# Kernel tuning notes

Measured on AMD Instinct MI355X. Metric: run time of the kernel, lower is better.

Reference implementation:

```python
import jax, jax.numpy as jnp
import numpy as np

N_NODES = 10000
N_EDGES = 320000
D = 128      # node/edge feature dim
H = 512      # MLP hidden width


def _mlp(x, W1, b1, W2, b2):
    return jax.nn.relu(x @ W1 + b1) @ W2 + b2


def setup_inputs() -> dict:
    key = jax.random.key(0)
    ks = jax.random.split(key, 8)
    s = lambda fan_in: 1.0 / np.sqrt(fan_in)
    return {
        "x": jax.random.normal(ks[0], (N_NODES, D), jnp.float32),
        "edge_index": jax.random.randint(ks[1], (2, N_EDGES), 0, N_NODES, jnp.int64),
        "edge_attr": jax.random.normal(ks[2], (N_EDGES, D), jnp.float32),
        "We1": jax.random.normal(ks[3], (3 * D, H), jnp.float32) * s(3 * D),
        "be1": jnp.zeros((H,), jnp.float32),
        "We2": jax.random.normal(ks[4], (H, D), jnp.float32) * s(H),
        "be2": jnp.zeros((D,), jnp.float32),
        "Wn1": jax.random.normal(ks[5], (2 * D, H), jnp.float32) * s(2 * D),
        "bn1": jnp.zeros((H,), jnp.float32),
        "Wn2": jax.random.normal(ks[6], (H, D), jnp.float32) * s(H),
        "bn2": jnp.zeros((D,), jnp.float32),
    }


def reference(x, edge_index, edge_attr, We1, be1, We2, be2, Wn1, bn1, Wn2, bn2):
    senders = edge_index[0]
    receivers = edge_index[1]
    # gather -> edge MLP
    edge_inputs = jnp.concatenate([x[senders], x[receivers], edge_attr], axis=-1)  # [E, 3D]
    updated_edge_attr = _mlp(edge_inputs, We1, be1, We2, be2)                      # [E, D]
    # scatter-add into receiving nodes
    aggregated = jax.ops.segment_sum(updated_edge_attr, receivers, num_segments=x.shape[0])  # [N, D]
    # node MLP
    node_inputs = jnp.concatenate([x, aggregated], axis=-1)                        # [N, 2D]
    updated_nodes = _mlp(node_inputs, Wn1, bn1, Wn2, bn2)                          # [N, D]
    return updated_nodes, updated_edge_attr
```

## Files before the change

kernel.cpp:

```cpp
#include <hip/hip_runtime.h>
#include <hip/hip_bf16.h>

#define N_NODES 10000
#define N_EDGES 320000
#define D 128
#define H 512

typedef __bf16 bf16x8 __attribute__((ext_vector_type(8)));
typedef float f32x4 __attribute__((ext_vector_type(4)));
typedef unsigned short u16x8 __attribute__((ext_vector_type(8)));

__device__ __forceinline__ unsigned short f2bf(float f) {
    union { float f; unsigned u; } v; v.f = f;
    unsigned r = v.u + 0x7fffu + ((v.u >> 16) & 1u);
    return (unsigned short)(r >> 16);
}

__global__ void cast_x_kernel(const float* __restrict__ x, unsigned short* __restrict__ xb) {
    int t = blockIdx.x * 256 + threadIdx.x;
    float4 v = reinterpret_cast<const float4*>(x)[t];
    ushort4 o;
    o.x = f2bf(v.x); o.y = f2bf(v.y); o.z = f2bf(v.z); o.w = f2bf(v.w);
    reinterpret_cast<ushort4*>(xb)[t] = o;
}

__global__ void swizzle_w_kernel(const float* __restrict__ W, unsigned short* __restrict__ out,
                                 int K, int Nn) {
    int t = blockIdx.x * 256 + threadIdx.x;
    int total = (K >> 5) * (Nn >> 4) * 64;
    if (t >= total) return;
    int lane = t & 63;
    int tile = t >> 6;
    int ntiles = Nn >> 4;
    int nt = tile % ntiles;
    int kt = tile / ntiles;
    int k0 = kt * 32 + (lane >> 4) * 8;
    int n  = nt * 16 + (lane & 15);
    unsigned short tmp[8];
#pragma unroll
    for (int j = 0; j < 8; ++j) tmp[j] = f2bf(W[(size_t)(k0 + j) * Nn + n]);
    ushort4* dst = reinterpret_cast<ushort4*>(out + (size_t)t * 8);
    dst[0] = *reinterpret_cast<ushort4*>(&tmp[0]);
    dst[1] = *reinterpret_cast<ushort4*>(&tmp[4]);
}

__global__ void hist_kernel(const int* __restrict__ eidx, int* __restrict__ deg) {
    int e = blockIdx.x * 256 + threadIdx.x;
    if (e < N_EDGES) atomicAdd(&deg[eidx[N_EDGES + e]], 1);
}

__global__ __launch_bounds__(1024) void scan_kernel(const int* __restrict__ deg,
                                                    int* __restrict__ rowstart,
                                                    int* __restrict__ cursor) {
    __shared__ int wsums[16];
    const int t = threadIdx.x;
    const int lane = t & 63, wv = t >> 6;
    const int base = t * 10;
    int loc[10];
    int s = 0;
#pragma unroll
    for (int i = 0; i < 10; ++i) {
        int v = (base + i < N_NODES) ? deg[base + i] : 0;
        loc[i] = s; s += v;
    }
    const int tot = s;
    int inc = tot;
#pragma unroll
    for (int d = 1; d < 64; d <<= 1) {
        int n = __shfl_up(inc, d, 64);
        if (lane >= d) inc += n;
    }
    if (lane == 63) wsums[wv] = inc;
    __syncthreads();
    if (t == 0) {
        int run = 0;
#pragma unroll
        for (int w = 0; w < 16; ++w) { int v = wsums[w]; wsums[w] = run; run += v; }
    }
    __syncthreads();
    const int off = wsums[wv] + inc - tot;
#pragma unroll
    for (int i = 0; i < 10; ++i) {
        int idx = base + i;
        if (idx < N_NODES) { int v = off + loc[i]; rowstart[idx] = v; cursor[idx] = v; }
    }
    if (t == 1023) rowstart[N_NODES] = off + tot;
}

__global__ void scatter_kernel(const int* __restrict__ eidx, int* __restrict__ cursor,
                               int* __restrict__ elist) {
    int e = blockIdx.x * 256 + threadIdx.x;
    if (e < N_EDGES) {
        int p = atomicAdd(&cursor[eidx[N_EDGES + e]], 1);
        elist[p] = e;
    }
}

__global__ __launch_bounds__(256) void agg_kernel(
    const float* __restrict__ out_edges,
    const int* __restrict__ rowstart,
    const int* __restrict__ elist,
    unsigned short* __restrict__ aggb)
{
    int node = blockIdx.x * 4 + (threadIdx.x >> 6);
    int lane = threadIdx.x & 63;
    int r0 = rowstart[node], r1 = rowstart[node + 1];
    float sx = 0.f, sy = 0.f;
    for (int j = r0; j < r1; ++j) {
        int e = elist[j];
        float2 v = *reinterpret_cast<const float2*>(&out_edges[(size_t)e * 128 + lane * 2]);
        sx += v.x; sy += v.y;
    }
    ushort2 o; o.x = f2bf(sx); o.y = f2bf(sy);
    *reinterpret_cast<ushort2*>(&aggb[(size_t)node * 128 + lane * 2]) = o;
}

__global__ __launch_bounds__(256, 2) void edge_mlp_kernel(
    const unsigned short* __restrict__ xb,
    const int* __restrict__ eidx,
    const float* __restrict__ edge_attr,
    const unsigned short* __restrict__ We1s,
    const float* __restrict__ be1,
    const unsigned short* __restrict__ We2s,
    const float* __restrict__ be2,
    float* __restrict__ out_edges)
{
    __shared__ unsigned short sA[64 * 392];
    unsigned short* const sH0 = sA;
    unsigned short* const sH1 = sA + 64 * 136;

    const int tid = threadIdx.x;
    const int wave = tid >> 6, lane = tid & 63;
    const int e0 = blockIdx.x * 64;
    const int l15 = lane & 15;
    const int q8 = (lane >> 4) * 8;

#pragma unroll
    for (int seg = 0; seg < 2; ++seg) {
        for (int c = tid; c < 1024; c += 256) {
            int row = c >> 4;
            int off = (c & 15) << 3;
            int e = e0 + row;
            int node = eidx[seg * N_EDGES + e];
            *reinterpret_cast<bf16x8*>(&sA[row * 392 + seg * 128 + off]) =
                *reinterpret_cast<const bf16x8*>(&xb[(size_t)node * 128 + off]);
        }
    }
    for (int c = tid; c < 1024; c += 256) {
        int row = c >> 4;
        int off = (c & 15) << 3;
        int e = e0 + row;
        const float4* src = reinterpret_cast<const float4*>(&edge_attr[(size_t)e * 128 + off]);
        float4 v0 = src[0], v1 = src[1];
        u16x8 o;
        o[0] = f2bf(v0.x); o[1] = f2bf(v0.y); o[2] = f2bf(v0.z); o[3] = f2bf(v0.w);
        o[4] = f2bf(v1.x); o[5] = f2bf(v1.y); o[6] = f2bf(v1.z); o[7] = f2bf(v1.w);
        *reinterpret_cast<u16x8*>(&sA[row * 392 + 256 + off]) = o;
    }
    __syncthreads();

    f32x4 acc1[8][4];
#pragma unroll
    for (int j = 0; j < 8; ++j)
#pragma unroll
        for (int mt = 0; mt < 4; ++mt) acc1[j][mt] = (f32x4){0.f, 0.f, 0.f, 0.f};
    f32x4 acc2[2][4];
#pragma unroll
    for (int nn = 0; nn < 2; ++nn)
#pragma unroll
        for (int mt = 0; mt < 4; ++mt) acc2[nn][mt] = (f32x4){0.f, 0.f, 0.f, 0.f};

#pragma unroll 2
    for (int kt = 0; kt < 12; ++kt) {
        bf16x8 a[4];
#pragma unroll
        for (int mt = 0; mt < 4; ++mt)
            a[mt] = *reinterpret_cast<const bf16x8*>(&sA[(mt * 16 + l15) * 392 + kt * 32 + q8]);
#pragma unroll
        for (int j = 0; j < 8; ++j) {
            int ntile = (j >> 1) * 8 + wave * 2 + (j & 1);
            bf16x8 b = *reinterpret_cast<const bf16x8*>(
                &We1s[(((size_t)kt * 32 + ntile) * 64 + lane) * 8]);
#pragma unroll
            for (int mt = 0; mt < 4; ++mt)
                acc1[j][mt] = __builtin_amdgcn_mfma_f32_16x16x32_bf16(a[mt], b, acc1[j][mt], 0, 0, 0);
        }
    }

#define WRITE_H(hh, dst, B1)                                                  \
    {                                                                         \
        _Pragma("unroll")                                                     \
        for (int nn = 0; nn < 2; ++nn) {                                      \
            int cc = (wave * 2 + nn) * 16 + l15;                              \
            float bias = (B1)[(hh) * 128 + cc];                               \
            _Pragma("unroll")                                                 \
            for (int mt = 0; mt < 4; ++mt)                                    \
                _Pragma("unroll")                                             \
                for (int r = 0; r < 4; ++r) {                                 \
                    float v = acc1[(hh) * 2 + nn][mt][r] + bias;              \
                    v = v > 0.f ? v : 0.f;                                    \
                    int row = mt * 16 + (lane >> 4) * 4 + r;                  \
                    (dst)[row * 136 + cc] = f2bf(v);                          \
                }                                                             \
        }                                                                     \
    }

#define GEMM2_CHUNK(hh, src, W2)                                              \
    {                                                                         \
        _Pragma("unroll")                                                     \
        for (int kt = 0; kt < 4; ++kt) {                                      \
            bf16x8 a[4];                                                      \
            _Pragma("unroll")                                                 \
            for (int mt = 0; mt < 4; ++mt)                                    \
                a[mt] = *reinterpret_cast<const bf16x8*>(                     \
                    &(src)[(mt * 16 + l15) * 136 + kt * 32 + q8]);            \
            _Pragma("unroll")                                                 \
            for (int nn = 0; nn < 2; ++nn) {                                  \
                int ntile = wave * 2 + nn;                                    \
                bf16x8 b = *reinterpret_cast<const bf16x8*>(                  \
                    &(W2)[(((size_t)((hh) * 4 + kt) * 8 + ntile) * 64 + lane) * 8]); \
                _Pragma("unroll")                                             \
                for (int mt = 0; mt < 4; ++mt)                                \
                    acc2[nn][mt] = __builtin_amdgcn_mfma_f32_16x16x32_bf16(   \
                        a[mt], b, acc2[nn][mt], 0, 0, 0);                     \
            }                                                                 \
        }                                                                     \
    }

    __syncthreads();
    WRITE_H(0, sH0, be1);
    __syncthreads();
#pragma unroll
    for (int h = 0; h < 4; ++h) {
        unsigned short* const cur = (h & 1) ? sH1 : sH0;
        unsigned short* const nxt = (h & 1) ? sH0 : sH1;
        if (h < 3) WRITE_H(h + 1, nxt, be1);
        GEMM2_CHUNK(h, cur, We2s);
        if (h < 3) __syncthreads();
    }

#pragma unroll
    for (int nn = 0; nn < 2; ++nn) {
        int cc = (wave * 2 + nn) * 16 + l15;
        float bias = be2[cc];
#pragma unroll
        for (int mt = 0; mt < 4; ++mt)
#pragma unroll
            for (int r = 0; r < 4; ++r) {
                int row = mt * 16 + (lane >> 4) * 4 + r;
                out_edges[(size_t)(e0 + row) * 128 + cc] = acc2[nn][mt][r] + bias;
            }
    }
}

__global__ __launch_bounds__(256, 2) void node_mlp_kernel(
    const unsigned short* __restrict__ xb,
    const unsigned short* __restrict__ aggb,
    const unsigned short* __restrict__ Wn1s,
    const float* __restrict__ bn1,
    const unsigned short* __restrict__ Wn2s,
    const float* __restrict__ bn2,
    float* __restrict__ out_nodes)
{
    __shared__ unsigned short sA[17408];
    unsigned short* const sH0 = sA;
    unsigned short* const sH1 = sA + 64 * 136;

    const int tid = threadIdx.x;
    const int wave = tid >> 6, lane = tid & 63;
    const int n0 = blockIdx.x * 64;
    const int l15 = lane & 15;
    const int q8 = (lane >> 4) * 8;

    for (int c = tid; c < 1024; c += 256) {
        int row = c >> 4;
        int off = (c & 15) << 3;
        int node = n0 + row;
        bf16x8 v = {};
        if (node < N_NODES)
            v = *reinterpret_cast<const bf16x8*>(&xb[(size_t)node * 128 + off]);
        *reinterpret_cast<bf16x8*>(&sA[row * 264 + off]) = v;
    }
    for (int c = tid; c < 1024; c += 256) {
        int row = c >> 4;
        int off = (c & 15) << 3;
        int node = n0 + row;
        bf16x8 v = {};
        if (node < N_NODES)
            v = *reinterpret_cast<const bf16x8*>(&aggb[(size_t)node * 128 + off]);
        *reinterpret_cast<bf16x8*>(&sA[row * 264 + 128 + off]) = v;
    }
    __syncthreads();

    f32x4 acc1[8][4];
#pragma unroll
    for (int j = 0; j < 8; ++j)
#pragma unroll
        for (int mt = 0; mt < 4; ++mt) acc1[j][mt] = (f32x4){0.f, 0.f, 0.f, 0.f};
    f32x4 acc2[2][4];
#pragma unroll
    for (int nn = 0; nn < 2; ++nn)
#pragma unroll
        for (int mt = 0; mt < 4; ++mt) acc2[nn][mt] = (f32x4){0.f, 0.f, 0.f, 0.f};

#pragma unroll 2
    for (int kt = 0; kt < 8; ++kt) {
        bf16x8 a[4];
#pragma unroll
        for (int mt = 0; mt < 4; ++mt)
            a[mt] = *reinterpret_cast<const bf16x8*>(&sA[(mt * 16 + l15) * 264 + kt * 32 + q8]);
#pragma unroll
        for (int j = 0; j < 8; ++j) {
            int ntile = (j >> 1) * 8 + wave * 2 + (j & 1);
            bf16x8 b = *reinterpret_cast<const bf16x8*>(
                &Wn1s[(((size_t)kt * 32 + ntile) * 64 + lane) * 8]);
#pragma unroll
            for (int mt = 0; mt < 4; ++mt)
                acc1[j][mt] = __builtin_amdgcn_mfma_f32_16x16x32_bf16(a[mt], b, acc1[j][mt], 0, 0, 0);
        }
    }

    __syncthreads();
    WRITE_H(0, sH0, bn1);
    __syncthreads();
#pragma unroll
    for (int h = 0; h < 4; ++h) {
        unsigned short* const cur = (h & 1) ? sH1 : sH0;
        unsigned short* const nxt = (h & 1) ? sH0 : sH1;
        if (h < 3) WRITE_H(h + 1, nxt, bn1);
        GEMM2_CHUNK(h, cur, Wn2s);
        if (h < 3) __syncthreads();
    }

#pragma unroll
    for (int nn = 0; nn < 2; ++nn) {
        int cc = (wave * 2 + nn) * 16 + l15;
        float bias = bn2[cc];
#pragma unroll
        for (int mt = 0; mt < 4; ++mt)
#pragma unroll
            for (int r = 0; r < 4; ++r) {
                int row = mt * 16 + (lane >> 4) * 4 + r;
                int node = n0 + row;
                if (node < N_NODES)
                    out_nodes[(size_t)node * 128 + cc] = acc2[nn][mt][r] + bias;
            }
    }
}

extern "C" void kernel_launch(void* const* d_in, const int* in_sizes, int n_in,
                              void* d_out, int out_size, void* d_ws, size_t ws_size,
                              hipStream_t stream) {
    const float* x         = (const float*)d_in[0];
    const int*   eidx      = (const int*)d_in[1];
    const float* edge_attr = (const float*)d_in[2];
    const float* We1       = (const float*)d_in[3];
    const float* be1       = (const float*)d_in[4];
    const float* We2       = (const float*)d_in[5];
    const float* be2       = (const float*)d_in[6];
    const float* Wn1       = (const float*)d_in[7];
    const float* bn1       = (const float*)d_in[8];
    const float* Wn2       = (const float*)d_in[9];
    const float* bn2       = (const float*)d_in[10];
    float* out = (float*)d_out;

    char* ws = (char*)d_ws;
    size_t off = 0;
    auto alloc = [&](size_t bytes) {
        void* p = ws + off;
        off += (bytes + 255) & ~(size_t)255;
        return p;
    };
    unsigned short* xb   = (unsigned short*)alloc((size_t)N_NODES * D * 2);
    unsigned short* We1s = (unsigned short*)alloc((size_t)384 * 512 * 2);
    unsigned short* We2s = (unsigned short*)alloc((size_t)512 * 128 * 2);
    unsigned short* Wn1s = (unsigned short*)alloc((size_t)256 * 512 * 2);
    unsigned short* Wn2s = (unsigned short*)alloc((size_t)512 * 128 * 2);
    unsigned short* aggb = (unsigned short*)alloc((size_t)N_NODES * D * 2);
    int* deg      = (int*)alloc((size_t)(N_NODES + 1) * 4);
    int* rowstart = (int*)alloc((size_t)(N_NODES + 1) * 4);
    int* cursor   = (int*)alloc((size_t)(N_NODES + 1) * 4);
    int* elist    = (int*)alloc((size_t)N_EDGES * 4);

    float* out_edges = out + (size_t)N_NODES * D;

    hipMemsetAsync(deg, 0, (size_t)N_NODES * sizeof(int), stream);
    cast_x_kernel<<<(N_NODES * D / 4 + 255) / 256, 256, 0, stream>>>(x, xb);
    swizzle_w_kernel<<<(12 * 32 * 64 + 255) / 256, 256, 0, stream>>>(We1, We1s, 384, 512);
    swizzle_w_kernel<<<(16 * 8 * 64 + 255) / 256, 256, 0, stream>>>(We2, We2s, 512, 128);
    swizzle_w_kernel<<<(8 * 32 * 64 + 255) / 256, 256, 0, stream>>>(Wn1, Wn1s, 256, 512);
    swizzle_w_kernel<<<(16 * 8 * 64 + 255) / 256, 256, 0, stream>>>(Wn2, Wn2s, 512, 128);

    hist_kernel<<<(N_EDGES + 255) / 256, 256, 0, stream>>>(eidx, deg);
    scan_kernel<<<1, 1024, 0, stream>>>(deg, rowstart, cursor);
    scatter_kernel<<<(N_EDGES + 255) / 256, 256, 0, stream>>>(eidx, cursor, elist);

    edge_mlp_kernel<<<N_EDGES / 64, 256, 0, stream>>>(
        xb, eidx, edge_attr, We1s, be1, We2s, be2, out_edges);
    agg_kernel<<<N_NODES / 4, 256, 0, stream>>>(out_edges, rowstart, elist, aggb);
    node_mlp_kernel<<<(N_NODES + 63) / 64, 256, 0, stream>>>(
        xb, aggb, Wn1s, bn1, Wn2s, bn2, out);
}
```

Baseline: 690.5 us.

## Double-buffer edge MLP K-tiles via async global-to-LDS loads with 128-edge blocks

The edge MLP kernel now uses 128-edge blocks of 512 threads, arranged as 2x4 waves, in place of 64-edge blocks of 256 threads. The first GEMM streams its A (gathered node features plus bf16-converted edge_attr) and B (We1 tiles) through double-buffered LDS, using global_load_lds for the bf16 parts and an XOR swizzle to avoid bank conflicts. This overlaps the gather and weight loads with the MFMA work, where before the whole 384-wide input row was staged up front and We1 was read straight from global memory. Output stores become nontemporal. The larger LDS footprint (80KB) and 512-thread blocks may lower occupancy, and the kernel now pays one barrier per K step.

```diff
diff --git a/kernel.cpp b/kernel.cpp
--- a/kernel.cpp
+++ b/kernel.cpp
@@ -115,7 +115,39 @@
     *reinterpret_cast<ushort2*>(&aggb[(size_t)node * 128 + lane * 2]) = o;
 }
 
-__global__ __launch_bounds__(256, 2) void edge_mlp_kernel(
+__device__ __forceinline__ void gld_lds16(const void* g, void* l) {
+    __builtin_amdgcn_global_load_lds((const __attribute__((address_space(1))) void*)g,
+                                     (__attribute__((address_space(3))) void*)l, 16, 0, 0);
+}
+
+__device__ __forceinline__ void stage_a(int kt, unsigned short* Abuf, int wave, int lane,
+                                        const unsigned short* aS, const unsigned short* aR,
+                                        const float* aE) {
+    if (kt < 8) {
+        const unsigned short* src = (kt < 4) ? (aS + kt * 32) : (aR + (kt - 4) * 32);
+        gld_lds16(src, Abuf + wave * 512);
+    } else {
+        const float* s = aE + (kt - 8) * 32;
+        float4 v0 = *reinterpret_cast<const float4*>(s);
+        float4 v1 = *reinterpret_cast<const float4*>(s + 4);
+        u16x8 o;
+        o[0] = f2bf(v0.x); o[1] = f2bf(v0.y); o[2] = f2bf(v0.z); o[3] = f2bf(v0.w);
+        o[4] = f2bf(v1.x); o[5] = f2bf(v1.y); o[6] = f2bf(v1.z); o[7] = f2bf(v1.w);
+        *reinterpret_cast<u16x8*>(Abuf + wave * 512 + lane * 8) = o;
+    }
+}
+
+__device__ __forceinline__ void stage_b(int kt, unsigned short* Bbuf, int wave, int lane,
+                                        const unsigned short* We1s) {
+#pragma unroll
+    for (int i = 0; i < 4; ++i) {
+        int c = wave * 4 + i;
+        const unsigned short* src = We1s + ((size_t)kt * 32 + c) * 512 + lane * 8;
+        gld_lds16(src, Bbuf + c * 512);
+    }
+}
+
+__global__ __launch_bounds__(512, 2) void edge_mlp_kernel(
     const unsigned short* __restrict__ xb,
     const int* __restrict__ eidx,
     const float* __restrict__ edge_attr,
@@ -125,39 +157,28 @@
     const float* __restrict__ be2,
     float* __restrict__ out_edges)
 {
-    __shared__ unsigned short sA[64 * 392];
-    unsigned short* const sH0 = sA;
-    unsigned short* const sH1 = sA + 64 * 136;
+    __shared__ unsigned short smem[40960];
+    unsigned short* const A0  = smem;
+    unsigned short* const A1  = smem + 4096;
+    unsigned short* const B0  = smem + 8192;
+    unsigned short* const B1  = smem + 24576;
+    unsigned short* const sH0 = smem + 4096;
+    unsigned short* const sH1 = smem + 21504;
 
     const int tid = threadIdx.x;
     const int wave = tid >> 6, lane = tid & 63;
-    const int e0 = blockIdx.x * 64;
+    const int wr = wave >> 2, wc = wave & 3;
     const int l15 = lane & 15;
-    const int q8 = (lane >> 4) * 8;
-
-#pragma unroll
-    for (int seg = 0; seg < 2; ++seg) {
-        for (int c = tid; c < 1024; c += 256) {
-            int row = c >> 4;
-            int off = (c & 15) << 3;
-            int e = e0 + row;
-            int node = eidx[seg * N_EDGES + e];
-            *reinterpret_cast<bf16x8*>(&sA[row * 392 + seg * 128 + off]) =
-                *reinterpret_cast<const bf16x8*>(&xb[(size_t)node * 128 + off]);
-        }
-    }
-    for (int c = tid; c < 1024; c += 256) {
-        int row = c >> 4;
-        int off = (c & 15) << 3;
-        int e = e0 + row;
-        const float4* src = reinterpret_cast<const float4*>(&edge_attr[(size_t)e * 128 + off]);
-        float4 v0 = src[0], v1 = src[1];
-        u16x8 o;
-        o[0] = f2bf(v0.x); o[1] = f2bf(v0.y); o[2] = f2bf(v0.z); o[3] = f2bf(v0.w);
-        o[4] = f2bf(v1.x); o[5] = f2bf(v1.y); o[6] = f2bf(v1.z); o[7] = f2bf(v1.w);
-        *reinterpret_cast<u16x8*>(&sA[row * 392 + 256 + off]) = o;
-    }
-    __syncthreads();
+    const int Q = lane >> 4;
+    const int e0 = blockIdx.x * 128;
+
+    const int rs = wave * 16 + (lane >> 2);
+    const int sq = (lane & 3) ^ (rs & 3);
+    const int nS = eidx[e0 + rs];
+    const int nR = eidx[N_EDGES + e0 + rs];
+    const unsigned short* aS = xb + (size_t)nS * 128 + sq * 8;
+    const unsigned short* aR = xb + (size_t)nR * 128 + sq * 8;
+    const float*          aE = edge_attr + (size_t)(e0 + rs) * 128 + sq * 8;
 
     f32x4 acc1[8][4];
 #pragma unroll
@@ -170,22 +191,95 @@
 #pragma unroll
         for (int mt = 0; mt < 4; ++mt) acc2[nn][mt] = (f32x4){0.f, 0.f, 0.f, 0.f};
 
-#pragma unroll 2
+    stage_a(0, A0, wave, lane, aS, aR, aE);
+    stage_b(0, B0, wave, lane, We1s);
+    __syncthreads();
+
+#pragma unroll
     for (int kt = 0; kt < 12; ++kt) {
+        unsigned short* const Ac = (kt & 1) ? A1 : A0;
+        unsigned short* const Bc = (kt & 1) ? B1 : B0;
+        if (kt < 11) {
+            stage_a(kt + 1, (kt & 1) ? A0 : A1, wave, lane, aS, aR, aE);
+            stage_b(kt + 1, (kt & 1) ? B0 : B1, wave, lane, We1s);
+        }
         bf16x8 a[4];
 #pragma unroll
-        for (int mt = 0; mt < 4; ++mt)
-            a[mt] = *reinterpret_cast<const bf16x8*>(&sA[(mt * 16 + l15) * 392 + kt * 32 + q8]);
+        for (int mt = 0; mt < 4; ++mt) {
+            int R = wr * 64 + mt * 16 + l15;
+            a[mt] = *reinterpret_cast<const bf16x8*>(&Ac[R * 32 + ((Q ^ (R & 3)) * 8)]);
+        }
 #pragma unroll
         for (int j = 0; j < 8; ++j) {
-            int ntile = (j >> 1) * 8 + wave * 2 + (j & 1);
-            bf16x8 b = *reinterpret_cast<const bf16x8*>(
-                &We1s[(((size_t)kt * 32 + ntile) * 64 + lane) * 8]);
+            int ntile = (j >> 1) * 8 + wc * 2 + (j & 1);
+            bf16x8 b = *reinterpret_cast<const bf16x8*>(&Bc[ntile * 512 + lane * 8]);
 #pragma unroll
             for (int mt = 0; mt < 4; ++mt)
                 acc1[j][mt] = __builtin_amdgcn_mfma_f32_16x16x32_bf16(a[mt], b, acc1[j][mt], 0, 0, 0);
         }
-    }
+        __syncthreads();
+    }
+
+#define EWRITE_H(hh, dst)                                                     \
+    {                                                                         \
+        _Pragma("unroll")                                                     \
+        for (int nn = 0; nn < 2; ++nn) {                                      \
+            int cc = (wc * 2 + nn) * 16 + l15;                                \
+            float bias = be1[(hh) * 128 + cc];                                \
+            _Pragma("unroll")                                                 \
+            for (int mt = 0; mt < 4; ++mt)                                    \
+                _Pragma("unroll")                                             \
+                for (int r = 0; r < 4; ++r) {                                 \
+                    float v = acc1[(hh) * 2 + nn][mt][r] + bias;              \
+                    v = v > 0.f ? v : 0.f;                                    \
+                    int row = wr * 64 + mt * 16 + (lane >> 4) * 4 + r;        \
+                    (dst)[row * 136 + cc] = f2bf(v);                          \
+                }                                                             \
+        }                                                                     \
+    }
+
+    EWRITE_H(0, sH0);
+    __syncthreads();
+#pragma unroll
+    for (int h = 0; h < 4; ++h) {
+        unsigned short* const cur = (h & 1) ? sH1 : sH0;
+        unsigned short* const nxt = (h & 1) ? sH0 : sH1;
+        if (h < 3) EWRITE_H(h + 1, nxt);
+#pragma unroll
+        for (int kt = 0; kt < 4; ++kt) {
+            bf16x8 a[4];
+#pragma unroll
+            for (int mt = 0; mt < 4; ++mt) {
+                int R = wr * 64 + mt * 16 + l15;
+                a[mt] = *reinterpret_cast<const bf16x8*>(&cur[R * 136 + kt * 32 + Q * 8]);
+            }
+#pragma unroll
+            for (int nn = 0; nn < 2; ++nn) {
+                int ntile = wc * 2 + nn;
+                bf16x8 b = *reinterpret_cast<const bf16x8*>(
+                    &We2s[(((size_t)(h * 4 + kt) * 8 + ntile) * 64 + lane) * 8]);
+#pragma unroll
+                for (int mt = 0; mt < 4; ++mt)
+                    acc2[nn][mt] = __builtin_amdgcn_mfma_f32_16x16x32_bf16(a[mt], b, acc2[nn][mt], 0, 0, 0);
+            }
+        }
+        if (h < 3) __syncthreads();
+    }
+
+#pragma unroll
+    for (int nn = 0; nn < 2; ++nn) {
+        int cc = (wc * 2 + nn) * 16 + l15;
+        float bias = be2[cc];
+#pragma unroll
+        for (int mt = 0; mt < 4; ++mt)
+#pragma unroll
+            for (int r = 0; r < 4; ++r) {
+                int row = wr * 64 + mt * 16 + (lane >> 4) * 4 + r;
+                __builtin_nontemporal_store(acc2[nn][mt][r] + bias,
+                                            &out_edges[(size_t)(e0 + row) * 128 + cc]);
+            }
+    }
+}
 
 #define WRITE_H(hh, dst, B1)                                                  \
     {                                                                         \
@@ -227,32 +321,6 @@
         }                                                                     \
     }
 
-    __syncthreads();
-    WRITE_H(0, sH0, be1);
-    __syncthreads();
-#pragma unroll
-    for (int h = 0; h < 4; ++h) {
-        unsigned short* const cur = (h & 1) ? sH1 : sH0;
-        unsigned short* const nxt = (h & 1) ? sH0 : sH1;
-        if (h < 3) WRITE_H(h + 1, nxt, be1);
-        GEMM2_CHUNK(h, cur, We2s);
-        if (h < 3) __syncthreads();
-    }
-
-#pragma unroll
-    for (int nn = 0; nn < 2; ++nn) {
-        int cc = (wave * 2 + nn) * 16 + l15;
-        float bias = be2[cc];
-#pragma unroll
-        for (int mt = 0; mt < 4; ++mt)
-#pragma unroll
-            for (int r = 0; r < 4; ++r) {
-                int row = mt * 16 + (lane >> 4) * 4 + r;
-                out_edges[(size_t)(e0 + row) * 128 + cc] = acc2[nn][mt][r] + bias;
-            }
-    }
-}
-
 __global__ __launch_bounds__(256, 2) void node_mlp_kernel(
     const unsigned short* __restrict__ xb,
     const unsigned short* __restrict__ aggb,
@@ -395,7 +463,7 @@
     scan_kernel<<<1, 1024, 0, stream>>>(deg, rowstart, cursor);
     scatter_kernel<<<(N_EDGES + 255) / 256, 256, 0, stream>>>(eidx, cursor, elist);
 
-    edge_mlp_kernel<<<N_EDGES / 64, 256, 0, stream>>>(
+    edge_mlp_kernel<<<N_EDGES / 128, 512, 0, stream>>>(
         xb, eidx, edge_attr, We1s, be1, We2s, be2, out_edges);
     agg_kernel<<<N_NODES / 4, 256, 0, stream>>>(out_edges, rowstart, elist, aggb);
     node_mlp_kernel<<<(N_NODES + 63) / 64, 256, 0, stream>>>(
```

After: 611.1 us. 11.5% less time.
